# Kernel optimization log

Measured on AMD Instinct MI355X. Metric: run time of the kernel, lower is better.

Reference implementation:

```python
import jax, jax.numpy as jnp
import numpy as np

NPOINT, RADIUS, NSAMPLE = 512, 0.2, 32
MLP = [64, 64, 128]
IN_CH = 67
EPS = 1e-5


def farthest_point_sample(xyz, npoint):
    # xyz: [B, N, 3] -> idx [B, npoint]. Deterministic start at index 0.
    B, N, _ = xyz.shape

    def step(carry, _):
        dist, far = carry  # dist [B,N], far [B]
        centroid = jnp.take_along_axis(xyz, far[:, None, None], axis=1)  # [B,1,3]
        d = jnp.sum((xyz - centroid) ** 2, axis=-1)  # [B,N]
        dist = jnp.minimum(dist, d)
        return (dist, jnp.argmax(dist, axis=-1).astype(jnp.int32)), far

    init = (jnp.full((B, N), 1e10, dtype=xyz.dtype), jnp.zeros((B,), jnp.int32))
    _, idxs = jax.lax.scan(step, init, None, length=npoint)
    return idxs.T  # [B, npoint]


def query_ball_point(radius, nsample, xyz, new_xyz):
    # xyz [B,N,3], new_xyz [B,S,3] -> idx [B,S,nsample]
    B, N, _ = xyz.shape
    sqr = jnp.sum((new_xyz[:, :, None, :] - xyz[:, None, :, :]) ** 2, axis=-1)  # [B,S,N]
    gidx = jnp.where(sqr > radius * radius, N, jnp.arange(N, dtype=jnp.int32))
    gidx = jnp.sort(gidx, axis=-1)[:, :, :nsample]
    first = gidx[:, :, :1]
    return jnp.where(gidx == N, first, gidx).astype(jnp.int32)


def gather_points(pts, idx):
    # pts [B,N,C], idx [B,...] -> [B,...,C]
    return jax.vmap(lambda p, i: p[i])(pts, idx)


def sample_and_group(npoint, radius, nsample, xyz, points):
    fps_idx = farthest_point_sample(xyz, npoint)          # [B,S]
    new_xyz = gather_points(xyz, fps_idx)                 # [B,S,3]
    idx = query_ball_point(radius, nsample, xyz, new_xyz)  # [B,S,K]
    grouped_xyz = gather_points(xyz, idx)                 # [B,S,K,3]
    grouped_xyz_norm = grouped_xyz - new_xyz[:, :, None, :]
    grouped_pts = gather_points(points, idx)              # [B,S,K,D]
    new_points = jnp.concatenate([grouped_xyz_norm, grouped_pts], axis=-1)  # [B,S,K,3+D]
    return new_xyz, new_points


def mlp_bn_relu(x, w, b, gamma, beta):
    # x [B,C,K,S]; 1x1 conv + training-mode BatchNorm2d + ReLU
    y = jnp.einsum('oc,bcks->boks', w, x) + b[None, :, None, None]
    mean = jnp.mean(y, axis=(0, 2, 3), keepdims=True)
    var = jnp.var(y, axis=(0, 2, 3), keepdims=True)
    y = (y - mean) * jax.lax.rsqrt(var + EPS)
    y = y * gamma[None, :, None, None] + beta[None, :, None, None]
    return jax.nn.relu(y)


def setup_inputs() -> dict:
    key = jax.random.key(0)
    ks = jax.random.split(key, 8)
    B, N, D = 16, 2048, 64
    inp = {
        'xyz': jax.random.normal(ks[0], (B, 3, N), jnp.float32),
        'points': jax.random.normal(ks[1], (B, D, N), jnp.float32),
    }
    last = IN_CH
    for i, out in enumerate(MLP):
        kw = jax.random.fold_in(ks[2], i)
        inp[f'w{i}'] = jax.random.normal(kw, (out, last), jnp.float32) * 0.05
        inp[f'b{i}'] = jnp.zeros((out,), jnp.float32)
        inp[f'g{i}'] = jnp.ones((out,), jnp.float32)
        inp[f'bt{i}'] = jnp.zeros((out,), jnp.float32)
        last = out
    return inp


def reference(xyz, points, w0, b0, g0, bt0, w1, b1, g1, bt1, w2, b2, g2, bt2):
    # xyz [B,3,N], points [B,D,N]
    xyz_t = jnp.transpose(xyz, (0, 2, 1))      # [B,N,3]
    pts_t = jnp.transpose(points, (0, 2, 1))   # [B,N,D]
    new_xyz, new_points = sample_and_group(NPOINT, RADIUS, NSAMPLE, xyz_t, pts_t)
    # [B,S,K,C] -> [B,C,K,S]
    x = jnp.transpose(new_points, (0, 3, 2, 1))
    for (w, b, g, bt) in ((w0, b0, g0, bt0), (w1, b1, g1, bt1), (w2, b2, g2, bt2)):
        x = mlp_bn_relu(x, w, b, g, bt)
    feature = jnp.max(x, axis=2)               # [B,C',S]
    new_xyz_out = jnp.transpose(new_xyz, (0, 2, 1))  # [B,3,S]
    return new_xyz_out, feature
```

## Files before the change

kernel.cpp:

```cpp
#include <hip/hip_runtime.h>
#include <hip/hip_bf16.h>
#include <stdint.h>

#define NB 16
#define NPT 2048
#define NS 512
#define NK 32
#define PTOT (NB*NS*NK)
#define C_IN 67
#define EPSV 1e-5f

typedef __attribute__((ext_vector_type(8))) short short8;
typedef __attribute__((ext_vector_type(4))) float floatx4;

#define WS_NEWXYZ 0
#define WS_ST     24576
#define WS_W1BF   27136
#define WS_W2BF   29184
#define WS_RAWMAX 33280
#define WS_PTS_TB 557568
#define WS_Y1     1606144
#define WS_Y2     9994752

__device__ __forceinline__ float bf2f(ushort u){ return __uint_as_float((uint32_t)u<<16); }
__device__ __forceinline__ ushort f2bf(float f){
  uint32_t u = __float_as_uint(f);
  return (ushort)((u + 0x7FFFu + ((u>>16)&1u)) >> 16);
}

template<int CTRL>
__device__ __forceinline__ double dppmax64f(double k){
  long long b = __double_as_longlong(k);
  int lo = (int)(uint32_t)b, hi = (int)(b>>32);
  int olo = __builtin_amdgcn_update_dpp(lo, lo, CTRL, 0xF, 0xF, false);
  int ohi = __builtin_amdgcn_update_dpp(hi, hi, CTRL, 0xF, 0xF, false);
  double o = __hiloint2double(ohi, olo);
  return fmax(o, k);
}
__device__ __forceinline__ unsigned long long u64max(unsigned long long a, unsigned long long b){ return a>b?a:b; }

__global__ __launch_bounds__(256) void prep_kernel(const float* __restrict__ xyz,
    float* __restrict__ nxyz, float* __restrict__ out0,
    const float* __restrict__ pts, ushort* __restrict__ pts_tb,
    const float* __restrict__ w1, const float* __restrict__ w2,
    ushort* __restrict__ w1b, ushort* __restrict__ w2b, float* __restrict__ st)
{
  __shared__ union {
    struct { float4 lc[NPT]; double warr[2][4]; int sel[NS]; } f;
    float tile[64][65];
  } sm;
  const int blk = blockIdx.x;
  const int tid = threadIdx.x;
  if (blk < 16){
    const int b = blk;
    const float* xb = xyz + (size_t)b*3*NPT;
    float px[8], py[8], pz[8], dist[8];
    uint32_t lo_[8];
    #pragma unroll
    for (int j=0;j<8;j++){
      int n = j*256 + tid;
      float x = xb[n], y = xb[NPT+n], z = xb[2*NPT+n];
      sm.f.lc[n] = make_float4(x,y,z,0.f);
      px[j]=x; py[j]=y; pz[j]=z; dist[j]=1e10f;
      lo_[j] = ~(uint32_t)n;
    }
    if (tid==0) sm.f.sel[0]=0;
    __syncthreads();
    float4 c0 = sm.f.lc[0];
    float cx = c0.x, cy = c0.y, cz = c0.z;
    const int lane = tid & 63, wid = tid >> 6;
    for (int t=1;t<NS;t++){
      double kk[8];
      #pragma unroll
      for (int j=0;j<8;j++){
        float dx = __fsub_rn(px[j], cx);
        float dy = __fsub_rn(py[j], cy);
        float dz = __fsub_rn(pz[j], cz);
        float d  = __fadd_rn(__fadd_rn(__fmul_rn(dx,dx),__fmul_rn(dy,dy)),__fmul_rn(dz,dz));
        float dd = fminf(dist[j], d);
        dist[j] = dd;
        kk[j] = __hiloint2double((int)__float_as_uint(dd), (int)lo_[j]);
      }
      double m0 = fmax(kk[0],kk[1]), m1 = fmax(kk[2],kk[3]);
      double m2 = fmax(kk[4],kk[5]), m3 = fmax(kk[6],kk[7]);
      double best = fmax(fmax(m0,m1), fmax(m2,m3));
      best = dppmax64f<0xB1>(best);
      best = dppmax64f<0x4E>(best);
      best = dppmax64f<0x124>(best);
      best = dppmax64f<0x128>(best);
      long long bb = __double_as_longlong(best);
      int bl = (int)(uint32_t)bb, bh = (int)(bb>>32);
      unsigned long long k0 = (((unsigned long long)(uint32_t)__builtin_amdgcn_readlane(bh, 0))<<32)  | (uint32_t)__builtin_amdgcn_readlane(bl, 0);
      unsigned long long k1 = (((unsigned long long)(uint32_t)__builtin_amdgcn_readlane(bh, 16))<<32) | (uint32_t)__builtin_amdgcn_readlane(bl, 16);
      unsigned long long k2 = (((unsigned long long)(uint32_t)__builtin_amdgcn_readlane(bh, 32))<<32) | (uint32_t)__builtin_amdgcn_readlane(bl, 32);
      unsigned long long k3 = (((unsigned long long)(uint32_t)__builtin_amdgcn_readlane(bh, 48))<<32) | (uint32_t)__builtin_amdgcn_readlane(bl, 48);
      unsigned long long kw = u64max(u64max(k0,k1), u64max(k2,k3));
      if (lane==0) sm.f.warr[t&1][wid] = __longlong_as_double((long long)kw);
      __syncthreads();
      double w0 = sm.f.warr[t&1][0], w1_ = sm.f.warr[t&1][1], w2_ = sm.f.warr[t&1][2], w3 = sm.f.warr[t&1][3];
      double f = fmax(fmax(w0,w1_), fmax(w2_,w3));
      int n = (int)(~(uint32_t)__double_as_longlong(f));
      float4 cc = sm.f.lc[n];
      cx = cc.x; cy = cc.y; cz = cc.z;
      if (tid==0) sm.f.sel[t]=n;
    }
    __syncthreads();
    for (int s = tid; s < NS; s += 256){
      int n = sm.f.sel[s];
      float4 cc = sm.f.lc[n];
      float* np_ = nxyz + ((size_t)b*NS + s)*3;
      np_[0]=cc.x; np_[1]=cc.y; np_[2]=cc.z;
      float* ob = out0 + (size_t)b*3*NS + s;
      ob[0]=cc.x; ob[NS]=cc.y; ob[2*NS]=cc.z;
    }
  } else if (blk < 528){
    const int t2 = blk - 16;
    const int b = t2 >> 5;
    const int n0 = (t2 & 31) * 64;
    const int lane = tid & 63;
    const int row4 = tid >> 6;
    const float* src = pts + (size_t)b*64*NPT;
    #pragma unroll
    for (int r=0; r<16; r++){
      int cc = r*4 + row4;
      sm.tile[cc][lane] = src[(size_t)cc*NPT + n0 + lane];
    }
    __syncthreads();
    ushort* dst = pts_tb + ((size_t)b*NPT + n0)*64;
    #pragma unroll
    for (int r=0; r<16; r++){
      int nn = r*4 + row4;
      dst[(size_t)nn*64 + lane] = f2bf(sm.tile[lane][nn]);
    }
  } else {
    for (int i = tid; i < 4096; i += 256) w1b[i] = f2bf(w1[i]);
    for (int i = tid; i < 8192; i += 256) w2b[i] = f2bf(w2[i]);
    for (int i = tid; i < 2560; i += 256) st[i] = 0.f;
  }
}

__global__ __launch_bounds__(256) void conv1_kernel(const float* __restrict__ xyz,
    const ushort* __restrict__ pts_tb, const float* __restrict__ nxyz,
    const float* __restrict__ Wt, const float* __restrict__ bias,
    ushort* __restrict__ y1)
{
  __shared__ int gq[8][NK];
  const int tid = threadIdx.x;
  const int wid = tid>>6, lane = tid&63;
  const int p0 = blockIdx.x*256;
  const int bs0 = p0 >> 5;
  const int b = p0 >> 14;
  const float* xb = xyz + (size_t)b*3*NPT;
  const float r2 = 0.2f*0.2f;
  for (int gi=0; gi<2; gi++){
    const int gl = wid*2 + gi;
    const float* c = nxyz + (size_t)(bs0+gl)*3;
    const float cx = c[0], cy = c[1], cz = c[2];
    int cnt = 0, first = 0;
    for (int ch=0; ch<NPT/64 && cnt<NK; ch++){
      int n = ch*64 + lane;
      float dx = __fsub_rn(cx, xb[n]);
      float dy = __fsub_rn(cy, xb[NPT+n]);
      float dz = __fsub_rn(cz, xb[2*NPT+n]);
      float d  = __fadd_rn(__fadd_rn(__fmul_rn(dx,dx),__fmul_rn(dy,dy)),__fmul_rn(dz,dz));
      bool in = (d <= r2);
      unsigned long long mask = __ballot(in);
      if (mask){
        if (cnt==0) first = ch*64 + (__ffsll((unsigned long long)mask)-1);
        if (in){
          int pos = cnt + __popcll(mask & ((1ull<<lane)-1ull));
          if (pos < NK) gq[gl][pos] = n;
        }
        cnt += __popcll(mask);
      }
    }
    if (cnt < NK && lane >= cnt && lane < NK) gq[gl][lane] = first;
  }
  __syncthreads();
  const int p = p0 + tid;
  const int bs = p >> 5;
  const int n = gq[tid>>5][tid&31];
  float x[C_IN];
  {
    const float* cc = nxyz + (size_t)bs*3;
    x[0] = xb[n]        - cc[0];
    x[1] = xb[NPT+n]    - cc[1];
    x[2] = xb[2*NPT+n]  - cc[2];
    const ushort* pr = pts_tb + ((size_t)b*NPT + n)*64;
    #pragma unroll
    for (int q=0;q<8;q++){
      short8 v = *(const short8*)(pr + q*8);
      #pragma unroll
      for (int j=0;j<8;j++) x[3+8*q+j] = bf2f((ushort)v[j]);
    }
  }
  ushort* yr = y1 + (size_t)p*64;
  #pragma unroll 1
  for (int o=0;o<64;o+=8){
    float a[8];
    #pragma unroll
    for (int k=0;k<8;k++) a[k] = bias[o+k];
    #pragma unroll
    for (int c=0;c<C_IN;c++){
      float xv = x[c];
      #pragma unroll
      for (int k=0;k<8;k++) a[k] = fmaf(Wt[(o+k)*C_IN+c], xv, a[k]);
    }
    short8 sv;
    #pragma unroll
    for (int k=0;k<8;k++) sv[k] = (short)f2bf(a[k]);
    *(short8*)(yr + o) = sv;
  }
}

__global__ __launch_bounds__(256) void stats64_kernel(const ushort* __restrict__ y,
                                                      float* __restrict__ stbase)
{
  const int wid = threadIdx.x>>6, lane = threadIdx.x&63;
  const int oct = lane & 7, pr = lane >> 3;
  const int p0 = blockIdx.x*1024 + wid*256;
  float s[8], s2[8];
  #pragma unroll
  for (int j=0;j<8;j++){ s[j]=0.f; s2[j]=0.f; }
  for (int it=0; it<32; it++){
    int p = p0 + it*8 + pr;
    short8 v = *(const short8*)(y + (size_t)p*64 + oct*8);
    #pragma unroll
    for (int j=0;j<8;j++){
      float f = bf2f((ushort)v[j]);
      s[j] += f; s2[j] = fmaf(f,f,s2[j]);
    }
  }
  #pragma unroll
  for (int off=8; off<64; off<<=1){
    #pragma unroll
    for (int j=0;j<8;j++){ s[j] += __shfl_xor(s[j],off,64); s2[j] += __shfl_xor(s2[j],off,64); }
  }
  __shared__ float sd[4][128];
  if (pr==0){
    #pragma unroll
    for (int j=0;j<8;j++){ sd[wid][oct*8+j] = s[j]; sd[wid][64+oct*8+j] = s2[j]; }
  }
  __syncthreads();
  int t = threadIdx.x;
  if (t < 128){
    float v = sd[0][t]+sd[1][t]+sd[2][t]+sd[3][t];
    int rep = blockIdx.x & 1;
    float* dst = (t<64) ? (stbase + rep*64 + t) : (stbase + 128 + rep*64 + (t-64));
    atomicAdd(dst, v);
  }
}

__global__ __launch_bounds__(256) void conv2_mfma(const ushort* __restrict__ yin,
    const float* __restrict__ st, const float* __restrict__ g0, const float* __restrict__ bt0,
    const ushort* __restrict__ Wb, const float* __restrict__ bias,
    ushort* __restrict__ yout)
{
  __shared__ float aAl[64], aBl[64];
  const int tid = threadIdx.x;
  if (tid < 64){
    float s = st[tid] + st[64+tid];
    float qv = st[128+tid] + st[192+tid];
    float mean = s * (1.f/PTOT);
    float var  = qv * (1.f/PTOT) - mean*mean;
    float a = g0[tid] * rsqrtf(var + EPSV);
    aAl[tid] = a;
    aBl[tid] = fmaf(-mean, a, bt0[tid]);
  }
  __syncthreads();
  const int wid = tid>>6, lane = tid&63;
  const int q = lane>>4, nn = lane&15;
  const int p0 = (blockIdx.x*4 + wid) * 32;
  float a_[2][8], b_[2][8];
  #pragma unroll
  for (int kh=0;kh<2;kh++)
    #pragma unroll
    for (int j=0;j<8;j++){
      a_[kh][j] = aAl[kh*32 + q*8 + j];
      b_[kh][j] = aBl[kh*32 + q*8 + j];
    }
  short8 Af[4][2];
  #pragma unroll
  for (int mt=0;mt<4;mt++)
    #pragma unroll
    for (int kh=0;kh<2;kh++)
      Af[mt][kh] = *(const short8*)(Wb + (mt*16 + nn)*64 + kh*32 + q*8);
  float bias_[4][4];
  #pragma unroll
  for (int mt=0;mt<4;mt++)
    #pragma unroll
    for (int r=0;r<4;r++) bias_[mt][r] = bias[mt*16 + q*4 + r];
  floatx4 z = {0.f,0.f,0.f,0.f};
  floatx4 acc[4][2];
  #pragma unroll
  for (int mt=0;mt<4;mt++){ acc[mt][0]=z; acc[mt][1]=z; }
  #pragma unroll
  for (int nt=0;nt<2;nt++){
    #pragma unroll
    for (int kh=0;kh<2;kh++){
      short8 raw = *(const short8*)(yin + (size_t)(p0 + nt*16 + nn)*64 + kh*32 + q*8);
      short8 bf;
      #pragma unroll
      for (int j=0;j<8;j++){
        float f = bf2f((ushort)raw[j]);
        f = fmaxf(fmaf(f, a_[kh][j], b_[kh][j]), 0.f);
        bf[j] = (short)f2bf(f);
      }
      #pragma unroll
      for (int mt=0;mt<4;mt++)
        acc[mt][nt] = __builtin_amdgcn_mfma_f32_16x16x32_bf16(Af[mt][kh], bf, acc[mt][nt], 0,0,0);
    }
  }
  #pragma unroll
  for (int nt=0;nt<2;nt++){
    int p = p0 + nt*16 + nn;
    #pragma unroll
    for (int mt=0;mt<4;mt++){
      float v0 = acc[mt][nt][0] + bias_[mt][0];
      float v1 = acc[mt][nt][1] + bias_[mt][1];
      float v2 = acc[mt][nt][2] + bias_[mt][2];
      float v3 = acc[mt][nt][3] + bias_[mt][3];
      uint2 w;
      w.x = (uint32_t)f2bf(v0) | ((uint32_t)f2bf(v1)<<16);
      w.y = (uint32_t)f2bf(v2) | ((uint32_t)f2bf(v3)<<16);
      *(uint2*)(yout + (size_t)p*64 + mt*16 + q*4) = w;
    }
  }
}

__global__ __launch_bounds__(256) void conv3_mfma(const ushort* __restrict__ yin,
    float* __restrict__ st, const float* __restrict__ g1, const float* __restrict__ bt1,
    const ushort* __restrict__ Wb, const float* __restrict__ bias,
    ushort* __restrict__ rawmax)
{
  __shared__ ushort tile[64*132];
  __shared__ float aAl[64], aBl[64];
  const int tid = threadIdx.x;
  if (tid < 64){
    float s = st[256+tid] + st[320+tid];
    float qv = st[384+tid] + st[448+tid];
    float mean = s * (1.f/PTOT);
    float var  = qv * (1.f/PTOT) - mean*mean;
    float a = g1[tid] * rsqrtf(var + EPSV);
    aAl[tid] = a;
    aBl[tid] = fmaf(-mean, a, bt1[tid]);
  }
  __syncthreads();
  const int wid = tid>>6, lane = tid&63;
  const int q = lane>>4, nn = lane&15;
  const int p0 = (blockIdx.x*4 + wid) * 16;
  float a_[2][8], b_[2][8];
  #pragma unroll
  for (int kh=0;kh<2;kh++)
    #pragma unroll
    for (int j=0;j<8;j++){
      a_[kh][j] = aAl[kh*32 + q*8 + j];
      b_[kh][j] = aBl[kh*32 + q*8 + j];
    }
  short8 bfr[2];
  #pragma unroll
  for (int kh=0;kh<2;kh++){
    short8 raw = *(const short8*)(yin + (size_t)(p0 + nn)*64 + kh*32 + q*8);
    short8 bf;
    #pragma unroll
    for (int j=0;j<8;j++){
      float f = bf2f((ushort)raw[j]);
      f = fmaxf(fmaf(f, a_[kh][j], b_[kh][j]), 0.f);
      bf[j] = (short)f2bf(f);
    }
    bfr[kh] = bf;
  }
  #pragma unroll 1
  for (int mh=0;mh<2;mh++){
    floatx4 z = {0.f,0.f,0.f,0.f};
    floatx4 acc[4];
    short8 Af[4][2];
    #pragma unroll
    for (int mt=0;mt<4;mt++){
      acc[mt]=z;
      #pragma unroll
      for (int kh=0;kh<2;kh++)
        Af[mt][kh] = *(const short8*)(Wb + ((mh*4+mt)*16 + nn)*64 + kh*32 + q*8);
    }
    #pragma unroll
    for (int kh=0;kh<2;kh++)
      #pragma unroll
      for (int mt=0;mt<4;mt++)
        acc[mt] = __builtin_amdgcn_mfma_f32_16x16x32_bf16(Af[mt][kh], bfr[kh], acc[mt], 0,0,0);
    #pragma unroll
    for (int mt=0;mt<4;mt++){
      int m0 = (mh*4+mt)*16;
      float v0 = acc[mt][0] + bias[m0 + q*4 + 0];
      float v1 = acc[mt][1] + bias[m0 + q*4 + 1];
      float v2 = acc[mt][2] + bias[m0 + q*4 + 2];
      float v3 = acc[mt][3] + bias[m0 + q*4 + 3];
      uint2 w;
      w.x = (uint32_t)f2bf(v0) | ((uint32_t)f2bf(v1)<<16);
      w.y = (uint32_t)f2bf(v2) | ((uint32_t)f2bf(v3)<<16);
      *(uint2*)&tile[(wid*16 + nn)*132 + m0 + q*4] = w;
    }
  }
  __syncthreads();
  const int c = tid >> 1, half = tid & 1;
  float s = 0.f, q2 = 0.f, mx = -1e30f;
  #pragma unroll 4
  for (int it=0; it<32; it++){
    float f = bf2f(tile[(half*32 + it)*132 + c]);
    s += f; q2 = fmaf(f,f,q2); mx = fmaxf(mx, f);
  }
  rawmax[(size_t)(blockIdx.x*2 + half)*128 + c] = f2bf(mx);
  s  += __shfl_xor(s, 1, 64);
  q2 += __shfl_xor(q2, 1, 64);
  if (half==0){
    int rep = blockIdx.x & 7;
    atomicAdd(&st[512  + rep*128 + c], s);
    atomicAdd(&st[1536 + rep*128 + c], q2);
  }
}

__global__ __launch_bounds__(256) void finalize_kernel(const ushort* __restrict__ rawmax,
    const float* __restrict__ st, const float* __restrict__ g2, const float* __restrict__ bt2,
    float* __restrict__ out)
{
  __shared__ float tile[64][65];
  __shared__ float aAl[128], aBl[128];
  const int tid = threadIdx.x;
  if (tid < 128){
    float s=0.f, qv=0.f;
    #pragma unroll
    for (int r=0;r<8;r++){ s += st[512 + r*128 + tid]; qv += st[1536 + r*128 + tid]; }
    float mean = s * (1.f/PTOT);
    float var  = qv * (1.f/PTOT) - mean*mean;
    float a = g2[tid] * rsqrtf(var + EPSV);
    aAl[tid] = a;
    aBl[tid] = fmaf(-mean, a, bt2[tid]);
  }
  __syncthreads();
  const int b  = blockIdx.x >> 4;
  const int ct = (blockIdx.x >> 3) & 1;
  const int stt = blockIdx.x & 7;
  const int c0 = ct*64, s0 = stt*64;
  const int lane = tid & 63, wid = tid >> 6;
  #pragma unroll
  for (int r=0;r<16;r++){
    int sl = r*4 + wid;
    tile[sl][lane] = bf2f(rawmax[((size_t)(b*512 + s0 + sl))*128 + c0 + lane]);
  }
  __syncthreads();
  #pragma unroll
  for (int r=0;r<16;r++){
    int cl = r*4 + wid;
    float a = aAl[c0+cl], bb = aBl[c0+cl];
    out[((size_t)(b*128 + c0 + cl))*512 + s0 + lane] = fmaxf(fmaf(tile[lane][cl], a, bb), 0.f);
  }
}

extern "C" void kernel_launch(void* const* d_in, const int* in_sizes, int n_in,
                              void* d_out, int out_size, void* d_ws, size_t ws_size,
                              hipStream_t stream) {
  const float* xyz = (const float*)d_in[0];
  const float* pts = (const float*)d_in[1];
  const float* w0  = (const float*)d_in[2];
  const float* b0  = (const float*)d_in[3];
  const float* g0  = (const float*)d_in[4];
  const float* bt0 = (const float*)d_in[5];
  const float* w1  = (const float*)d_in[6];
  const float* b1  = (const float*)d_in[7];
  const float* g1  = (const float*)d_in[8];
  const float* bt1 = (const float*)d_in[9];
  const float* w2  = (const float*)d_in[10];
  const float* b2  = (const float*)d_in[11];
  const float* g2  = (const float*)d_in[12];
  const float* bt2 = (const float*)d_in[13];
  float* out = (float*)d_out;
  float* ws  = (float*)d_ws;

  float* nxyz = ws + WS_NEWXYZ;
  float* st   = ws + WS_ST;
  ushort* w1b = (ushort*)(ws + WS_W1BF);
  ushort* w2b = (ushort*)(ws + WS_W2BF);
  ushort* rawmax = (ushort*)(ws + WS_RAWMAX);
  ushort* pts_tb = (ushort*)(ws + WS_PTS_TB);
  ushort* y1 = (ushort*)(ws + WS_Y1);
  ushort* y2 = (ushort*)(ws + WS_Y2);

  prep_kernel<<<529,256,0,stream>>>(xyz, nxyz, out, pts, pts_tb, w1, w2, w1b, w2b, st);
  conv1_kernel<<<PTOT/256,256,0,stream>>>(xyz, pts_tb, nxyz, w0, b0, y1);
  stats64_kernel<<<256,256,0,stream>>>(y1, st);
  conv2_mfma<<<2048,256,0,stream>>>(y1, st, g0, bt0, w1b, b1, y2);
  stats64_kernel<<<256,256,0,stream>>>(y2, st + 256);
  conv3_mfma<<<4096,256,0,stream>>>(y2, st, g1, bt1, w2b, b2, rawmax);
  finalize_kernel<<<256,256,0,stream>>>(rawmax, st, g2, bt2, out + NB*3*NS);
}
```

Before: 510.7 us.

## Fuse all stages into one cooperative persistent kernel with grid syncs

Replaces the seven separate kernel launches with a single cooperative mega-kernel that uses grid-wide syncs between phases: FPS/prep, ball query plus conv1, stats, conv2, stats, conv3, finalize. Conv1 is rewritten to use bf16 MFMA with a reordered, padded bf16 copy of w0 instead of the scalar fp32 loop. This removes launch gaps and the scalar conv1 cost. In exchange it adds grid-sync overhead, and a persistent grid capped at 1024 blocks may underutilize some phases while other blocks idle during the serial FPS phase.

```diff
diff --git a/kernel.cpp b/kernel.cpp
--- a/kernel.cpp
+++ b/kernel.cpp
@@ -1,13 +1,15 @@
 #include <hip/hip_runtime.h>
 #include <hip/hip_bf16.h>
+#include <hip/hip_cooperative_groups.h>
 #include <stdint.h>
+
+namespace cg = cooperative_groups;
 
 #define NB 16
 #define NPT 2048
 #define NS 512
 #define NK 32
 #define PTOT (NB*NS*NK)
-#define C_IN 67
 #define EPSV 1e-5f
 
 typedef __attribute__((ext_vector_type(8))) short short8;
@@ -17,10 +19,11 @@
 #define WS_ST     24576
 #define WS_W1BF   27136
 #define WS_W2BF   29184
-#define WS_RAWMAX 33280
-#define WS_PTS_TB 557568
-#define WS_Y1     1606144
-#define WS_Y2     9994752
+#define WS_W0R    33280
+#define WS_RAWMAX 36352
+#define WS_PTS_TB 560640
+#define WS_Y1     1609216
+#define WS_Y2     9997824
 
 __device__ __forceinline__ float bf2f(ushort u){ return __uint_as_float((uint32_t)u<<16); }
 __device__ __forceinline__ ushort f2bf(float f){
@@ -39,19 +42,76 @@
 }
 __device__ __forceinline__ unsigned long long u64max(unsigned long long a, unsigned long long b){ return a>b?a:b; }
 
-__global__ __launch_bounds__(256) void prep_kernel(const float* __restrict__ xyz,
-    float* __restrict__ nxyz, float* __restrict__ out0,
-    const float* __restrict__ pts, ushort* __restrict__ pts_tb,
-    const float* __restrict__ w1, const float* __restrict__ w2,
-    ushort* __restrict__ w1b, ushort* __restrict__ w2b, float* __restrict__ st)
+__device__ __forceinline__ void stats64_phase(const ushort* __restrict__ y, float* __restrict__ stbase,
+                                              char* smraw, int blk, int G, int tid)
 {
-  __shared__ union {
-    struct { float4 lc[NPT]; double warr[2][4]; int sel[NS]; } f;
-    float tile[64][65];
-  } sm;
-  const int blk = blockIdx.x;
-  const int tid = threadIdx.x;
+  const int wid = tid>>6, lane = tid&63;
+  const int oct = lane & 7, pr = lane >> 3;
+  float* sd = (float*)smraw;
+  for (int u = blk; u < 256; u += G){
+    __syncthreads();
+    const int p0 = u*1024 + wid*256;
+    float s[8], s2[8];
+    #pragma unroll
+    for (int j=0;j<8;j++){ s[j]=0.f; s2[j]=0.f; }
+    for (int it=0; it<32; it++){
+      int p = p0 + it*8 + pr;
+      short8 v = *(const short8*)(y + (size_t)p*64 + oct*8);
+      #pragma unroll
+      for (int j=0;j<8;j++){
+        float f = bf2f((ushort)v[j]);
+        s[j] += f; s2[j] = fmaf(f,f,s2[j]);
+      }
+    }
+    #pragma unroll
+    for (int off=8; off<64; off<<=1){
+      #pragma unroll
+      for (int j=0;j<8;j++){ s[j] += __shfl_xor(s[j],off,64); s2[j] += __shfl_xor(s2[j],off,64); }
+    }
+    if (pr==0){
+      #pragma unroll
+      for (int j=0;j<8;j++){ sd[wid*128 + oct*8+j] = s[j]; sd[wid*128 + 64+oct*8+j] = s2[j]; }
+    }
+    __syncthreads();
+    if (tid < 128){
+      float v = sd[tid]+sd[128+tid]+sd[256+tid]+sd[384+tid];
+      int rep = u & 1;
+      float* dst = (tid<64) ? (stbase + rep*64 + tid) : (stbase + 128 + rep*64 + (tid-64));
+      atomicAdd(dst, v);
+    }
+  }
+}
+
+__global__ __launch_bounds__(256) void mega_kernel(
+    const float* __restrict__ xyz, const float* __restrict__ pts,
+    const float* __restrict__ w0, const float* __restrict__ b0,
+    const float* __restrict__ g0v, const float* __restrict__ bt0,
+    const float* __restrict__ w1, const float* __restrict__ b1,
+    const float* __restrict__ g1v, const float* __restrict__ bt1,
+    const float* __restrict__ w2, const float* __restrict__ b2,
+    const float* __restrict__ g2v, const float* __restrict__ bt2,
+    float* __restrict__ out, float* __restrict__ ws)
+{
+  __shared__ __align__(16) char smraw[34944];
+  cg::grid_group gridg = cg::this_grid();
+  const int blk = blockIdx.x, tid = threadIdx.x;
+  const int lane = tid & 63, wid = tid >> 6;
+  const int G = (int)gridDim.x;
+
+  float* nxyz = ws + WS_NEWXYZ;
+  float* st   = ws + WS_ST;
+  ushort* w1b = (ushort*)(ws + WS_W1BF);
+  ushort* w2b = (ushort*)(ws + WS_W2BF);
+  ushort* w0r = (ushort*)(ws + WS_W0R);
+  ushort* rawmax = (ushort*)(ws + WS_RAWMAX);
+  ushort* pts_tb = (ushort*)(ws + WS_PTS_TB);
+  ushort* y1 = (ushort*)(ws + WS_Y1);
+  ushort* y2 = (ushort*)(ws + WS_Y2);
+
   if (blk < 16){
+    float4* lc = (float4*)smraw;
+    double* warr = (double*)(smraw + 32768);
+    int* sel = (int*)(smraw + 32832);
     const int b = blk;
     const float* xb = xyz + (size_t)b*3*NPT;
     float px[8], py[8], pz[8], dist[8];
@@ -60,15 +120,14 @@
     for (int j=0;j<8;j++){
       int n = j*256 + tid;
       float x = xb[n], y = xb[NPT+n], z = xb[2*NPT+n];
-      sm.f.lc[n] = make_float4(x,y,z,0.f);
+      lc[n] = make_float4(x,y,z,0.f);
       px[j]=x; py[j]=y; pz[j]=z; dist[j]=1e10f;
       lo_[j] = ~(uint32_t)n;
     }
-    if (tid==0) sm.f.sel[0]=0;
+    if (tid==0) sel[0]=0;
     __syncthreads();
-    float4 c0 = sm.f.lc[0];
+    float4 c0 = lc[0];
     float cx = c0.x, cy = c0.y, cz = c0.z;
-    const int lane = tid & 63, wid = tid >> 6;
     for (int t=1;t<NS;t++){
       double kk[8];
       #pragma unroll
@@ -95,363 +154,345 @@
       unsigned long long k2 = (((unsigned long long)(uint32_t)__builtin_amdgcn_readlane(bh, 32))<<32) | (uint32_t)__builtin_amdgcn_readlane(bl, 32);
       unsigned long long k3 = (((unsigned long long)(uint32_t)__builtin_amdgcn_readlane(bh, 48))<<32) | (uint32_t)__builtin_amdgcn_readlane(bl, 48);
       unsigned long long kw = u64max(u64max(k0,k1), u64max(k2,k3));
-      if (lane==0) sm.f.warr[t&1][wid] = __longlong_as_double((long long)kw);
+      if (lane==0) warr[(t&1)*4 + wid] = __longlong_as_double((long long)kw);
       __syncthreads();
-      double w0 = sm.f.warr[t&1][0], w1_ = sm.f.warr[t&1][1], w2_ = sm.f.warr[t&1][2], w3 = sm.f.warr[t&1][3];
-      double f = fmax(fmax(w0,w1_), fmax(w2_,w3));
+      double w0_ = warr[(t&1)*4+0], w1_ = warr[(t&1)*4+1], w2_ = warr[(t&1)*4+2], w3_ = warr[(t&1)*4+3];
+      double f = fmax(fmax(w0_,w1_), fmax(w2_,w3_));
       int n = (int)(~(uint32_t)__double_as_longlong(f));
-      float4 cc = sm.f.lc[n];
+      float4 cc = lc[n];
       cx = cc.x; cy = cc.y; cz = cc.z;
-      if (tid==0) sm.f.sel[t]=n;
+      if (tid==0) sel[t]=n;
     }
     __syncthreads();
     for (int s = tid; s < NS; s += 256){
-      int n = sm.f.sel[s];
-      float4 cc = sm.f.lc[n];
+      int n = sel[s];
+      float4 cc = lc[n];
       float* np_ = nxyz + ((size_t)b*NS + s)*3;
       np_[0]=cc.x; np_[1]=cc.y; np_[2]=cc.z;
-      float* ob = out0 + (size_t)b*3*NS + s;
+      float* ob = out + (size_t)b*3*NS + s;
       ob[0]=cc.x; ob[NS]=cc.y; ob[2*NS]=cc.z;
     }
-  } else if (blk < 528){
-    const int t2 = blk - 16;
-    const int b = t2 >> 5;
-    const int n0 = (t2 & 31) * 64;
-    const int lane = tid & 63;
-    const int row4 = tid >> 6;
-    const float* src = pts + (size_t)b*64*NPT;
-    #pragma unroll
-    for (int r=0; r<16; r++){
-      int cc = r*4 + row4;
-      sm.tile[cc][lane] = src[(size_t)cc*NPT + n0 + lane];
+  } else {
+    float (*tile)[65] = (float(*)[65])smraw;
+    for (int u = blk-16; u < 513; u += G-16){
+      __syncthreads();
+      if (u < 512){
+        const int b = u >> 5;
+        const int n0 = (u & 31) * 64;
+        const int row4 = tid >> 6;
+        const float* src = pts + (size_t)b*64*NPT;
+        #pragma unroll
+        for (int r=0; r<16; r++){
+          int cc = r*4 + row4;
+          tile[cc][lane] = src[(size_t)cc*NPT + n0 + lane];
+        }
+        __syncthreads();
+        ushort* dst = pts_tb + ((size_t)b*NPT + n0)*64;
+        #pragma unroll
+        for (int r=0; r<16; r++){
+          int nn2 = r*4 + row4;
+          dst[(size_t)nn2*64 + lane] = f2bf(tile[lane][nn2]);
+        }
+      } else {
+        for (int i = tid; i < 4096; i += 256) w1b[i] = f2bf(w1[i]);
+        for (int i = tid; i < 8192; i += 256) w2b[i] = f2bf(w2[i]);
+        for (int i = tid; i < 2560; i += 256) st[i] = 0.f;
+        for (int i = tid; i < 6144; i += 256){
+          int o = i / 96, k = i - o*96;
+          float v = (k < 64) ? w0[o*67 + 3 + k] : ((k < 67) ? w0[o*67 + (k-64)] : 0.f);
+          w0r[i] = f2bf(v);
+        }
+      }
+    }
+  }
+  gridg.sync();
+
+  {
+    int* gqrow = (int*)smraw + wid*32;
+    const int q = lane>>4, nn = lane&15;
+    for (int g = blk*4 + wid; g < NB*NS; g += G*4){
+      const int b = g >> 9;
+      const float* xb = xyz + (size_t)b*3*NPT;
+      const float* cgp = nxyz + (size_t)g*3;
+      const float cx = cgp[0], cy = cgp[1], cz = cgp[2];
+      {
+        const float r2 = 0.2f*0.2f;
+        int cnt = 0, first = 0;
+        for (int ch=0; ch<NPT/64 && cnt<NK; ch++){
+          int n = ch*64 + lane;
+          float dx = __fsub_rn(cx, xb[n]);
+          float dy = __fsub_rn(cy, xb[NPT+n]);
+          float dz = __fsub_rn(cz, xb[2*NPT+n]);
+          float d  = __fadd_rn(__fadd_rn(__fmul_rn(dx,dx),__fmul_rn(dy,dy)),__fmul_rn(dz,dz));
+          bool in = (d <= r2);
+          unsigned long long mask = __ballot(in);
+          if (mask){
+            if (cnt==0) first = ch*64 + (__ffsll((unsigned long long)mask)-1);
+            if (in){
+              int pos = cnt + __popcll(mask & ((1ull<<lane)-1ull));
+              if (pos < NK) gqrow[pos] = n;
+            }
+            cnt += __popcll(mask);
+          }
+        }
+        if (cnt < NK && lane >= cnt && lane < NK) gqrow[lane] = first;
+      }
+      int n0 = gqrow[nn], n1 = gqrow[16+nn];
+      float dx0 = xb[n0]-cx, dy0 = xb[NPT+n0]-cy, dz0 = xb[2*NPT+n0]-cz;
+      float dx1 = xb[n1]-cx, dy1 = xb[NPT+n1]-cy, dz1 = xb[2*NPT+n1]-cz;
+      floatx4 z4 = {0.f,0.f,0.f,0.f};
+      floatx4 acc[4][2];
+      #pragma unroll
+      for (int mt=0;mt<4;mt++){ acc[mt][0]=z4; acc[mt][1]=z4; }
+      const ushort* pr0 = pts_tb + ((size_t)b*NPT + n0)*64;
+      const ushort* pr1 = pts_tb + ((size_t)b*NPT + n1)*64;
+      #pragma unroll
+      for (int kh=0; kh<2; kh++){
+        short8 B0 = *(const short8*)(pr0 + kh*32 + q*8);
+        short8 B1 = *(const short8*)(pr1 + kh*32 + q*8);
+        #pragma unroll
+        for (int mt=0; mt<4; mt++){
+          short8 A = *(const short8*)(w0r + (mt*16+nn)*96 + kh*32 + q*8);
+          acc[mt][0] = __builtin_amdgcn_mfma_f32_16x16x32_bf16(A, B0, acc[mt][0], 0,0,0);
+          acc[mt][1] = __builtin_amdgcn_mfma_f32_16x16x32_bf16(A, B1, acc[mt][1], 0,0,0);
+        }
+      }
+      {
+        short8 B0 = {0,0,0,0,0,0,0,0}, B1 = {0,0,0,0,0,0,0,0};
+        if (q==0){
+          B0[0]=(short)f2bf(dx0); B0[1]=(short)f2bf(dy0); B0[2]=(short)f2bf(dz0);
+          B1[0]=(short)f2bf(dx1); B1[1]=(short)f2bf(dy1); B1[2]=(short)f2bf(dz1);
+        }
+        #pragma unroll
+        for (int mt=0; mt<4; mt++){
+          short8 A = *(const short8*)(w0r + (mt*16+nn)*96 + 64 + q*8);
+          acc[mt][0] = __builtin_amdgcn_mfma_f32_16x16x32_bf16(A, B0, acc[mt][0], 0,0,0);
+          acc[mt][1] = __builtin_amdgcn_mfma_f32_16x16x32_bf16(A, B1, acc[mt][1], 0,0,0);
+        }
+      }
+      #pragma unroll
+      for (int nt=0; nt<2; nt++){
+        int p = g*32 + nt*16 + nn;
+        #pragma unroll
+        for (int mt=0; mt<4; mt++){
+          float v0 = acc[mt][nt][0] + b0[mt*16 + q*4 + 0];
+          float v1 = acc[mt][nt][1] + b0[mt*16 + q*4 + 1];
+          float v2 = acc[mt][nt][2] + b0[mt*16 + q*4 + 2];
+          float v3 = acc[mt][nt][3] + b0[mt*16 + q*4 + 3];
+          uint2 wv;
+          wv.x = (uint32_t)f2bf(v0) | ((uint32_t)f2bf(v1)<<16);
+          wv.y = (uint32_t)f2bf(v2) | ((uint32_t)f2bf(v3)<<16);
+          *(uint2*)(y1 + (size_t)p*64 + mt*16 + q*4) = wv;
+        }
+      }
+    }
+  }
+  gridg.sync();
+
+  stats64_phase(y1, st, smraw, blk, G, tid);
+  gridg.sync();
+
+  {
+    float* aAl = (float*)smraw;
+    float* aBl = (float*)(smraw + 256);
+    if (tid < 64){
+      float s = st[tid] + st[64+tid];
+      float qv = st[128+tid] + st[192+tid];
+      float mean = s * (1.f/PTOT);
+      float var  = qv * (1.f/PTOT) - mean*mean;
+      float a = g0v[tid] * rsqrtf(var + EPSV);
+      aAl[tid] = a;
+      aBl[tid] = fmaf(-mean, a, bt0[tid]);
     }
     __syncthreads();
-    ushort* dst = pts_tb + ((size_t)b*NPT + n0)*64;
-    #pragma unroll
-    for (int r=0; r<16; r++){
-      int nn = r*4 + row4;
-      dst[(size_t)nn*64 + lane] = f2bf(sm.tile[lane][nn]);
-    }
-  } else {
-    for (int i = tid; i < 4096; i += 256) w1b[i] = f2bf(w1[i]);
-    for (int i = tid; i < 8192; i += 256) w2b[i] = f2bf(w2[i]);
-    for (int i = tid; i < 2560; i += 256) st[i] = 0.f;
+    const int q = lane>>4, nn = lane&15;
+    float a_[2][8], b_[2][8];
+    #pragma unroll
+    for (int kh=0;kh<2;kh++)
+      #pragma unroll
+      for (int j=0;j<8;j++){
+        a_[kh][j] = aAl[kh*32 + q*8 + j];
+        b_[kh][j] = aBl[kh*32 + q*8 + j];
+      }
+    short8 Af[4][2];
+    #pragma unroll
+    for (int mt=0;mt<4;mt++)
+      #pragma unroll
+      for (int kh=0;kh<2;kh++)
+        Af[mt][kh] = *(const short8*)(w1b + (mt*16 + nn)*64 + kh*32 + q*8);
+    float bias_[4][4];
+    #pragma unroll
+    for (int mt=0;mt<4;mt++)
+      #pragma unroll
+      for (int r=0;r<4;r++) bias_[mt][r] = b1[mt*16 + q*4 + r];
+    for (int u = blk; u < 2048; u += G){
+      const int p0 = (u*4 + wid) * 32;
+      floatx4 z4 = {0.f,0.f,0.f,0.f};
+      floatx4 acc[4][2];
+      #pragma unroll
+      for (int mt=0;mt<4;mt++){ acc[mt][0]=z4; acc[mt][1]=z4; }
+      #pragma unroll
+      for (int nt=0;nt<2;nt++){
+        #pragma unroll
+        for (int kh=0;kh<2;kh++){
+          short8 raw = *(const short8*)(y1 + (size_t)(p0 + nt*16 + nn)*64 + kh*32 + q*8);
+          short8 bf;
+          #pragma unroll
+          for (int j=0;j<8;j++){
+            float f = bf2f((ushort)raw[j]);
+            f = fmaxf(fmaf(f, a_[kh][j], b_[kh][j]), 0.f);
+            bf[j] = (short)f2bf(f);
+          }
+          #pragma unroll
+          for (int mt=0;mt<4;mt++)
+            acc[mt][nt] = __builtin_amdgcn_mfma_f32_16x16x32_bf16(Af[mt][kh], bf, acc[mt][nt], 0,0,0);
+        }
+      }
+      #pragma unroll
+      for (int nt=0;nt<2;nt++){
+        int p = p0 + nt*16 + nn;
+        #pragma unroll
+        for (int mt=0;mt<4;mt++){
+          float v0 = acc[mt][nt][0] + bias_[mt][0];
+          float v1 = acc[mt][nt][1] + bias_[mt][1];
+          float v2 = acc[mt][nt][2] + bias_[mt][2];
+          float v3 = acc[mt][nt][3] + bias_[mt][3];
+          uint2 wv;
+          wv.x = (uint32_t)f2bf(v0) | ((uint32_t)f2bf(v1)<<16);
+          wv.y = (uint32_t)f2bf(v2) | ((uint32_t)f2bf(v3)<<16);
+          *(uint2*)(y2 + (size_t)p*64 + mt*16 + q*4) = wv;
+        }
+      }
+    }
   }
-}
-
-__global__ __launch_bounds__(256) void conv1_kernel(const float* __restrict__ xyz,
-    const ushort* __restrict__ pts_tb, const float* __restrict__ nxyz,
-    const float* __restrict__ Wt, const float* __restrict__ bias,
-    ushort* __restrict__ y1)
-{
-  __shared__ int gq[8][NK];
-  const int tid = threadIdx.x;
-  const int wid = tid>>6, lane = tid&63;
-  const int p0 = blockIdx.x*256;
-  const int bs0 = p0 >> 5;
-  const int b = p0 >> 14;
-  const float* xb = xyz + (size_t)b*3*NPT;
-  const float r2 = 0.2f*0.2f;
-  for (int gi=0; gi<2; gi++){
-    const int gl = wid*2 + gi;
-    const float* c = nxyz + (size_t)(bs0+gl)*3;
-    const float cx = c[0], cy = c[1], cz = c[2];
-    int cnt = 0, first = 0;
-    for (int ch=0; ch<NPT/64 && cnt<NK; ch++){
-      int n = ch*64 + lane;
-      float dx = __fsub_rn(cx, xb[n]);
-      float dy = __fsub_rn(cy, xb[NPT+n]);
-      float dz = __fsub_rn(cz, xb[2*NPT+n]);
-      float d  = __fadd_rn(__fadd_rn(__fmul_rn(dx,dx),__fmul_rn(dy,dy)),__fmul_rn(dz,dz));
-      bool in = (d <= r2);
-      unsigned long long mask = __ballot(in);
-      if (mask){
-        if (cnt==0) first = ch*64 + (__ffsll((unsigned long long)mask)-1);
-        if (in){
-          int pos = cnt + __popcll(mask & ((1ull<<lane)-1ull));
-          if (pos < NK) gq[gl][pos] = n;
-        }
-        cnt += __popcll(mask);
-      }
-    }
-    if (cnt < NK && lane >= cnt && lane < NK) gq[gl][lane] = first;
+  gridg.sync();
+
+  stats64_phase(y2, st + 256, smraw, blk, G, tid);
+  gridg.sync();
+
+  {
+    ushort* tile = (ushort*)smraw;
+    float* aAl = (float*)(smraw + 16896);
+    float* aBl = (float*)(smraw + 17152);
+    if (tid < 64){
+      float s = st[256+tid] + st[320+tid];
+      float qv = st[384+tid] + st[448+tid];
+      float mean = s * (1.f/PTOT);
+      float var  = qv * (1.f/PTOT) - mean*mean;
+      float a = g1v[tid] * rsqrtf(var + EPSV);
+      aAl[tid] = a;
+      aBl[tid] = fmaf(-mean, a, bt1[tid]);
+    }
+    __syncthreads();
+    const int q = lane>>4, nn = lane&15;
+    float a_[2][8], b_[2][8];
+    #pragma unroll
+    for (int kh=0;kh<2;kh++)
+      #pragma unroll
+      for (int j=0;j<8;j++){
+        a_[kh][j] = aAl[kh*32 + q*8 + j];
+        b_[kh][j] = aBl[kh*32 + q*8 + j];
+      }
+    for (int u = blk; u < 4096; u += G){
+      __syncthreads();
+      const int p0 = (u*4 + wid) * 16;
+      short8 bfr[2];
+      #pragma unroll
+      for (int kh=0;kh<2;kh++){
+        short8 raw = *(const short8*)(y2 + (size_t)(p0 + nn)*64 + kh*32 + q*8);
+        short8 bf;
+        #pragma unroll
+        for (int j=0;j<8;j++){
+          float f = bf2f((ushort)raw[j]);
+          f = fmaxf(fmaf(f, a_[kh][j], b_[kh][j]), 0.f);
+          bf[j] = (short)f2bf(f);
+        }
+        bfr[kh] = bf;
+      }
+      #pragma unroll 1
+      for (int mh=0;mh<2;mh++){
+        floatx4 z4 = {0.f,0.f,0.f,0.f};
+        floatx4 acc[4];
+        short8 Af[4][2];
+        #pragma unroll
+        for (int mt=0;mt<4;mt++){
+          acc[mt]=z4;
+          #pragma unroll
+          for (int kh=0;kh<2;kh++)
+            Af[mt][kh] = *(const short8*)(w2b + ((mh*4+mt)*16 + nn)*64 + kh*32 + q*8);
+        }
+        #pragma unroll
+        for (int kh=0;kh<2;kh++)
+          #pragma unroll
+          for (int mt=0;mt<4;mt++)
+            acc[mt] = __builtin_amdgcn_mfma_f32_16x16x32_bf16(Af[mt][kh], bfr[kh], acc[mt], 0,0,0);
+        #pragma unroll
+        for (int mt=0;mt<4;mt++){
+          int m0 = (mh*4+mt)*16;
+          float v0 = acc[mt][0] + b2[m0 + q*4 + 0];
+          float v1 = acc[mt][1] + b2[m0 + q*4 + 1];
+          float v2 = acc[mt][2] + b2[m0 + q*4 + 2];
+          float v3 = acc[mt][3] + b2[m0 + q*4 + 3];
+          uint2 wv;
+          wv.x = (uint32_t)f2bf(v0) | ((uint32_t)f2bf(v1)<<16);
+          wv.y = (uint32_t)f2bf(v2) | ((uint32_t)f2bf(v3)<<16);
+          *(uint2*)&tile[(wid*16 + nn)*132 + m0 + q*4] = wv;
+        }
+      }
+      __syncthreads();
+      const int c = tid >> 1, half = tid & 1;
+      float s = 0.f, q2 = 0.f, mx = -1e30f;
+      #pragma unroll 4
+      for (int it=0; it<32; it++){
+        float f = bf2f(tile[(half*32 + it)*132 + c]);
+        s += f; q2 = fmaf(f,f,q2); mx = fmaxf(mx, f);
+      }
+      rawmax[(size_t)(u*2 + half)*128 + c] = f2bf(mx);
+      s  += __shfl_xor(s, 1, 64);
+      q2 += __shfl_xor(q2, 1, 64);
+      if (half==0){
+        int rep = u & 7;
+        atomicAdd(&st[512  + rep*128 + c], s);
+        atomicAdd(&st[1536 + rep*128 + c], q2);
+      }
+    }
   }
-  __syncthreads();
-  const int p = p0 + tid;
-  const int bs = p >> 5;
-  const int n = gq[tid>>5][tid&31];
-  float x[C_IN];
+  gridg.sync();
+
   {
-    const float* cc = nxyz + (size_t)bs*3;
-    x[0] = xb[n]        - cc[0];
-    x[1] = xb[NPT+n]    - cc[1];
-    x[2] = xb[2*NPT+n]  - cc[2];
-    const ushort* pr = pts_tb + ((size_t)b*NPT + n)*64;
-    #pragma unroll
-    for (int q=0;q<8;q++){
-      short8 v = *(const short8*)(pr + q*8);
-      #pragma unroll
-      for (int j=0;j<8;j++) x[3+8*q+j] = bf2f((ushort)v[j]);
-    }
-  }
-  ushort* yr = y1 + (size_t)p*64;
-  #pragma unroll 1
-  for (int o=0;o<64;o+=8){
-    float a[8];
-    #pragma unroll
-    for (int k=0;k<8;k++) a[k] = bias[o+k];
-    #pragma unroll
-    for (int c=0;c<C_IN;c++){
-      float xv = x[c];
-      #pragma unroll
-      for (int k=0;k<8;k++) a[k] = fmaf(Wt[(o+k)*C_IN+c], xv, a[k]);
-    }
-    short8 sv;
-    #pragma unroll
-    for (int k=0;k<8;k++) sv[k] = (short)f2bf(a[k]);
-    *(short8*)(yr + o) = sv;
-  }
-}
-
-__global__ __launch_bounds__(256) void stats64_kernel(const ushort* __restrict__ y,
-                                                      float* __restrict__ stbase)
-{
-  const int wid = threadIdx.x>>6, lane = threadIdx.x&63;
-  const int oct = lane & 7, pr = lane >> 3;
-  const int p0 = blockIdx.x*1024 + wid*256;
-  float s[8], s2[8];
-  #pragma unroll
-  for (int j=0;j<8;j++){ s[j]=0.f; s2[j]=0.f; }
-  for (int it=0; it<32; it++){
-    int p = p0 + it*8 + pr;
-    short8 v = *(const short8*)(y + (size_t)p*64 + oct*8);
-    #pragma unroll
-    for (int j=0;j<8;j++){
-      float f = bf2f((ushort)v[j]);
-      s[j] += f; s2[j] = fmaf(f,f,s2[j]);
-    }
-  }
-  #pragma unroll
-  for (int off=8; off<64; off<<=1){
-    #pragma unroll
-    for (int j=0;j<8;j++){ s[j] += __shfl_xor(s[j],off,64); s2[j] += __shfl_xor(s2[j],off,64); }
-  }
-  __shared__ float sd[4][128];
-  if (pr==0){
-    #pragma unroll
-    for (int j=0;j<8;j++){ sd[wid][oct*8+j] = s[j]; sd[wid][64+oct*8+j] = s2[j]; }
-  }
-  __syncthreads();
-  int t = threadIdx.x;
-  if (t < 128){
-    float v = sd[0][t]+sd[1][t]+sd[2][t]+sd[3][t];
-    int rep = blockIdx.x & 1;
-    float* dst = (t<64) ? (stbase + rep*64 + t) : (stbase + 128 + rep*64 + (t-64));
-    atomicAdd(dst, v);
-  }
-}
-
-__global__ __launch_bounds__(256) void conv2_mfma(const ushort* __restrict__ yin,
-    const float* __restrict__ st, const float* __restrict__ g0, const float* __restrict__ bt0,
-    const ushort* __restrict__ Wb, const float* __restrict__ bias,
-    ushort* __restrict__ yout)
-{
-  __shared__ float aAl[64], aBl[64];
-  const int tid = threadIdx.x;
-  if (tid < 64){
-    float s = st[tid] + st[64+tid];
-    float qv = st[128+tid] + st[192+tid];
-    float mean = s * (1.f/PTOT);
-    float var  = qv * (1.f/PTOT) - mean*mean;
-    float a = g0[tid] * rsqrtf(var + EPSV);
-    aAl[tid] = a;
-    aBl[tid] = fmaf(-mean, a, bt0[tid]);
-  }
-  __syncthreads();
-  const int wid = tid>>6, lane = tid&63;
-  const int q = lane>>4, nn = lane&15;
-  const int p0 = (blockIdx.x*4 + wid) * 32;
-  float a_[2][8], b_[2][8];
-  #pragma unroll
-  for (int kh=0;kh<2;kh++)
-    #pragma unroll
-    for (int j=0;j<8;j++){
-      a_[kh][j] = aAl[kh*32 + q*8 + j];
-      b_[kh][j] = aBl[kh*32 + q*8 + j];
-    }
-  short8 Af[4][2];
-  #pragma unroll
-  for (int mt=0;mt<4;mt++)
-    #pragma unroll
-    for (int kh=0;kh<2;kh++)
-      Af[mt][kh] = *(const short8*)(Wb + (mt*16 + nn)*64 + kh*32 + q*8);
-  float bias_[4][4];
-  #pragma unroll
-  for (int mt=0;mt<4;mt++)
-    #pragma unroll
-    for (int r=0;r<4;r++) bias_[mt][r] = bias[mt*16 + q*4 + r];
-  floatx4 z = {0.f,0.f,0.f,0.f};
-  floatx4 acc[4][2];
-  #pragma unroll
-  for (int mt=0;mt<4;mt++){ acc[mt][0]=z; acc[mt][1]=z; }
-  #pragma unroll
-  for (int nt=0;nt<2;nt++){
-    #pragma unroll
-    for (int kh=0;kh<2;kh++){
-      short8 raw = *(const short8*)(yin + (size_t)(p0 + nt*16 + nn)*64 + kh*32 + q*8);
-      short8 bf;
-      #pragma unroll
-      for (int j=0;j<8;j++){
-        float f = bf2f((ushort)raw[j]);
-        f = fmaxf(fmaf(f, a_[kh][j], b_[kh][j]), 0.f);
-        bf[j] = (short)f2bf(f);
-      }
-      #pragma unroll
-      for (int mt=0;mt<4;mt++)
-        acc[mt][nt] = __builtin_amdgcn_mfma_f32_16x16x32_bf16(Af[mt][kh], bf, acc[mt][nt], 0,0,0);
-    }
-  }
-  #pragma unroll
-  for (int nt=0;nt<2;nt++){
-    int p = p0 + nt*16 + nn;
-    #pragma unroll
-    for (int mt=0;mt<4;mt++){
-      float v0 = acc[mt][nt][0] + bias_[mt][0];
-      float v1 = acc[mt][nt][1] + bias_[mt][1];
-      float v2 = acc[mt][nt][2] + bias_[mt][2];
-      float v3 = acc[mt][nt][3] + bias_[mt][3];
-      uint2 w;
-      w.x = (uint32_t)f2bf(v0) | ((uint32_t)f2bf(v1)<<16);
-      w.y = (uint32_t)f2bf(v2) | ((uint32_t)f2bf(v3)<<16);
-      *(uint2*)(yout + (size_t)p*64 + mt*16 + q*4) = w;
-    }
-  }
-}
-
-__global__ __launch_bounds__(256) void conv3_mfma(const ushort* __restrict__ yin,
-    float* __restrict__ st, const float* __restrict__ g1, const float* __restrict__ bt1,
-    const ushort* __restrict__ Wb, const float* __restrict__ bias,
-    ushort* __restrict__ rawmax)
-{
-  __shared__ ushort tile[64*132];
-  __shared__ float aAl[64], aBl[64];
-  const int tid = threadIdx.x;
-  if (tid < 64){
-    float s = st[256+tid] + st[320+tid];
-    float qv = st[384+tid] + st[448+tid];
-    float mean = s * (1.f/PTOT);
-    float var  = qv * (1.f/PTOT) - mean*mean;
-    float a = g1[tid] * rsqrtf(var + EPSV);
-    aAl[tid] = a;
-    aBl[tid] = fmaf(-mean, a, bt1[tid]);
-  }
-  __syncthreads();
-  const int wid = tid>>6, lane = tid&63;
-  const int q = lane>>4, nn = lane&15;
-  const int p0 = (blockIdx.x*4 + wid) * 16;
-  float a_[2][8], b_[2][8];
-  #pragma unroll
-  for (int kh=0;kh<2;kh++)
-    #pragma unroll
-    for (int j=0;j<8;j++){
-      a_[kh][j] = aAl[kh*32 + q*8 + j];
-      b_[kh][j] = aBl[kh*32 + q*8 + j];
-    }
-  short8 bfr[2];
-  #pragma unroll
-  for (int kh=0;kh<2;kh++){
-    short8 raw = *(const short8*)(yin + (size_t)(p0 + nn)*64 + kh*32 + q*8);
-    short8 bf;
-    #pragma unroll
-    for (int j=0;j<8;j++){
-      float f = bf2f((ushort)raw[j]);
-      f = fmaxf(fmaf(f, a_[kh][j], b_[kh][j]), 0.f);
-      bf[j] = (short)f2bf(f);
-    }
-    bfr[kh] = bf;
-  }
-  #pragma unroll 1
-  for (int mh=0;mh<2;mh++){
-    floatx4 z = {0.f,0.f,0.f,0.f};
-    floatx4 acc[4];
-    short8 Af[4][2];
-    #pragma unroll
-    for (int mt=0;mt<4;mt++){
-      acc[mt]=z;
-      #pragma unroll
-      for (int kh=0;kh<2;kh++)
-        Af[mt][kh] = *(const short8*)(Wb + ((mh*4+mt)*16 + nn)*64 + kh*32 + q*8);
-    }
-    #pragma unroll
-    for (int kh=0;kh<2;kh++)
-      #pragma unroll
-      for (int mt=0;mt<4;mt++)
-        acc[mt] = __builtin_amdgcn_mfma_f32_16x16x32_bf16(Af[mt][kh], bfr[kh], acc[mt], 0,0,0);
-    #pragma unroll
-    for (int mt=0;mt<4;mt++){
-      int m0 = (mh*4+mt)*16;
-      float v0 = acc[mt][0] + bias[m0 + q*4 + 0];
-      float v1 = acc[mt][1] + bias[m0 + q*4 + 1];
-      float v2 = acc[mt][2] + bias[m0 + q*4 + 2];
-      float v3 = acc[mt][3] + bias[m0 + q*4 + 3];
-      uint2 w;
-      w.x = (uint32_t)f2bf(v0) | ((uint32_t)f2bf(v1)<<16);
-      w.y = (uint32_t)f2bf(v2) | ((uint32_t)f2bf(v3)<<16);
-      *(uint2*)&tile[(wid*16 + nn)*132 + m0 + q*4] = w;
-    }
-  }
-  __syncthreads();
-  const int c = tid >> 1, half = tid & 1;
-  float s = 0.f, q2 = 0.f, mx = -1e30f;
-  #pragma unroll 4
-  for (int it=0; it<32; it++){
-    float f = bf2f(tile[(half*32 + it)*132 + c]);
-    s += f; q2 = fmaf(f,f,q2); mx = fmaxf(mx, f);
-  }
-  rawmax[(size_t)(blockIdx.x*2 + half)*128 + c] = f2bf(mx);
-  s  += __shfl_xor(s, 1, 64);
-  q2 += __shfl_xor(q2, 1, 64);
-  if (half==0){
-    int rep = blockIdx.x & 7;
-    atomicAdd(&st[512  + rep*128 + c], s);
-    atomicAdd(&st[1536 + rep*128 + c], q2);
-  }
-}
-
-__global__ __launch_bounds__(256) void finalize_kernel(const ushort* __restrict__ rawmax,
-    const float* __restrict__ st, const float* __restrict__ g2, const float* __restrict__ bt2,
-    float* __restrict__ out)
-{
-  __shared__ float tile[64][65];
-  __shared__ float aAl[128], aBl[128];
-  const int tid = threadIdx.x;
-  if (tid < 128){
-    float s=0.f, qv=0.f;
-    #pragma unroll
-    for (int r=0;r<8;r++){ s += st[512 + r*128 + tid]; qv += st[1536 + r*128 + tid]; }
-    float mean = s * (1.f/PTOT);
-    float var  = qv * (1.f/PTOT) - mean*mean;
-    float a = g2[tid] * rsqrtf(var + EPSV);
-    aAl[tid] = a;
-    aBl[tid] = fmaf(-mean, a, bt2[tid]);
-  }
-  __syncthreads();
-  const int b  = blockIdx.x >> 4;
-  const int ct = (blockIdx.x >> 3) & 1;
-  const int stt = blockIdx.x & 7;
-  const int c0 = ct*64, s0 = stt*64;
-  const int lane = tid & 63, wid = tid >> 6;
-  #pragma unroll
-  for (int r=0;r<16;r++){
-    int sl = r*4 + wid;
-    tile[sl][lane] = bf2f(rawmax[((size_t)(b*512 + s0 + sl))*128 + c0 + lane]);
-  }
-  __syncthreads();
-  #pragma unroll
-  for (int r=0;r<16;r++){
-    int cl = r*4 + wid;
-    float a = aAl[c0+cl], bb = aBl[c0+cl];
-    out[((size_t)(b*128 + c0 + cl))*512 + s0 + lane] = fmaxf(fmaf(tile[lane][cl], a, bb), 0.f);
+    float (*tile)[65] = (float(*)[65])smraw;
+    float* aAl = (float*)(smraw + 16640);
+    float* aBl = (float*)(smraw + 17152);
+    if (tid < 128){
+      float s=0.f, qv=0.f;
+      #pragma unroll
+      for (int r=0;r<8;r++){ s += st[512 + r*128 + tid]; qv += st[1536 + r*128 + tid]; }
+      float mean = s * (1.f/PTOT);
+      float var  = qv * (1.f/PTOT) - mean*mean;
+      float a = g2v[tid] * rsqrtf(var + EPSV);
+      aAl[tid] = a;
+      aBl[tid] = fmaf(-mean, a, bt2[tid]);
+    }
+    float* outf = out + NB*3*NS;
+    for (int u = blk; u < 256; u += G){
+      __syncthreads();
+      const int b  = u >> 4;
+      const int ct = (u >> 3) & 1;
+      const int stt = u & 7;
+      const int c0 = ct*64, s0 = stt*64;
+      #pragma unroll
+      for (int r=0;r<16;r++){
+        int sl = r*4 + wid;
+        tile[sl][lane] = bf2f(rawmax[((size_t)(b*512 + s0 + sl))*128 + c0 + lane]);
+      }
+      __syncthreads();
+      #pragma unroll
+      for (int r=0;r<16;r++){
+        int cl = r*4 + wid;
+        float a = aAl[c0+cl], bb = aBl[c0+cl];
+        outf[((size_t)(b*128 + c0 + cl))*512 + s0 + lane] = fmaxf(fmaf(tile[lane][cl], a, bb), 0.f);
+      }
+    }
   }
 }
 
@@ -475,20 +516,16 @@
   float* out = (float*)d_out;
   float* ws  = (float*)d_ws;
 
-  float* nxyz = ws + WS_NEWXYZ;
-  float* st   = ws + WS_ST;
-  ushort* w1b = (ushort*)(ws + WS_W1BF);
-  ushort* w2b = (ushort*)(ws + WS_W2BF);
-  ushort* rawmax = (ushort*)(ws + WS_RAWMAX);
-  ushort* pts_tb = (ushort*)(ws + WS_PTS_TB);
-  ushort* y1 = (ushort*)(ws + WS_Y1);
-  ushort* y2 = (ushort*)(ws + WS_Y2);
-
-  prep_kernel<<<529,256,0,stream>>>(xyz, nxyz, out, pts, pts_tb, w1, w2, w1b, w2b, st);
-  conv1_kernel<<<PTOT/256,256,0,stream>>>(xyz, pts_tb, nxyz, w0, b0, y1);
-  stats64_kernel<<<256,256,0,stream>>>(y1, st);
-  conv2_mfma<<<2048,256,0,stream>>>(y1, st, g0, bt0, w1b, b1, y2);
-  stats64_kernel<<<256,256,0,stream>>>(y2, st + 256);
-  conv3_mfma<<<4096,256,0,stream>>>(y2, st, g1, bt1, w2b, b2, rawmax);
-  finalize_kernel<<<256,256,0,stream>>>(rawmax, st, g2, bt2, out + NB*3*NS);
+  int nb = 0;
+  if (hipOccupancyMaxActiveBlocksPerMultiprocessor(&nb, (const void*)mega_kernel, 256, 0) != hipSuccess || nb < 1)
+    nb = 1;
+  int grid = nb * 256;
+  if (grid > 1024) grid = 1024;
+
+  void* args[] = { (void*)&xyz, (void*)&pts,
+                   (void*)&w0, (void*)&b0, (void*)&g0, (void*)&bt0,
+                   (void*)&w1, (void*)&b1, (void*)&g1, (void*)&bt1,
+                   (void*)&w2, (void*)&b2, (void*)&g2, (void*)&bt2,
+                   (void*)&out, (void*)&ws };
+  hipLaunchCooperativeKernel((void*)mega_kernel, dim3(grid), dim3(256), args, 0, stream);
 }
```

Result: slower. 686.1 us (+34.3%).
